# Performance work log

Hardware: AMD Instinct MI355X
Metric: run time of the kernel (lower is better)

## Reference

```python
import jax, jax.numpy as jnp
import numpy as np

B = 16384
D = 1024          # in_features
R = 64            # low_rank
E = 4             # num_experts
L = 3             # layer_num


def setup_inputs() -> dict:
    key = jax.random.key(0)
    ks = jax.random.split(key, 6)
    # xavier-normal-ish scales
    s_uv = (2.0 / (D + R)) ** 0.5
    s_c = (2.0 / (R + R)) ** 0.5
    s_g = (2.0 / (D + 1)) ** 0.5
    return {
        "inputs": jax.random.normal(ks[0], (B, D), dtype=jnp.float32),
        "U": jax.random.normal(ks[1], (L, E, D, R), dtype=jnp.float32) * s_uv,
        "V": jax.random.normal(ks[2], (L, E, D, R), dtype=jnp.float32) * s_uv,
        "C": jax.random.normal(ks[3], (L, E, R, R), dtype=jnp.float32) * s_c,
        "gate_w": jax.random.normal(ks[4], (E, D), dtype=jnp.float32) * s_g,
        "bias": jnp.zeros((L, D), dtype=jnp.float32),
    }


def reference(inputs, U, V, C, gate_w, bias):
    x0 = inputs                                  # [B, D]
    x_l = x0
    for i in range(L):
        # gating: per-expert Linear(d,1) on x_l -> [B, E], softmax over experts
        gates = jax.nn.softmax(x_l @ gate_w.T, axis=1)        # [B, E]
        # v_x = tanh(V_e^T x_l) for all experts at once
        v = jnp.tanh(jnp.einsum('bd,edr->ber', x_l, V[i]))    # [B, E, R]
        v = jnp.tanh(jnp.einsum('ers,bes->ber', C[i], v))     # [B, E, R]
        uv = jnp.einsum('edr,ber->bed', U[i], v)              # [B, E, D]
        dot = x0[:, None, :] * (uv + bias[i][None, None, :])  # [B, E, D]
        moe_out = jnp.einsum('bed,be->bd', dot, gates)        # [B, D]
        x_l = moe_out + x_l
    return x_l
```

## Files before the change

kernel.cpp:

```cpp
#include <hip/hip_runtime.h>
#include <math.h>

#define BB 16384
#define DD 1024
#define RR 64
#define EE 4
#define ER 256
#define LL 3

#define LDM 72

typedef __bf16 bf16x8 __attribute__((ext_vector_type(8)));
typedef float f32x4 __attribute__((ext_vector_type(4)));
typedef unsigned short us;

static __device__ inline us f2b(float f) {
    union { float f; unsigned u; } c; c.f = f;
    return (us)((c.u + 0x7FFF + ((c.u >> 16) & 1)) >> 16);
}
static __device__ inline float b2f(us v) {
    union { unsigned u; float f; } c; c.u = ((unsigned)v) << 16;
    return c.f;
}
static __device__ inline float fast_tanh(float x) {
    float t = __expf(2.f * x);
    return 1.f - 2.f / (t + 1.f);
}
static __device__ __forceinline__ void ld_lds16(const us* g, us* l) {
    __builtin_amdgcn_global_load_lds((const __attribute__((address_space(1))) void*)g,
                                     (__attribute__((address_space(3))) void*)l, 16, 0, 0);
}

__global__ __launch_bounds__(256) void convF2B(const float* __restrict__ s, us* __restrict__ d) {
    int f = (blockIdx.x * 256 + threadIdx.x) * 4;
    float4 v = *(const float4*)&s[f];
    *(ushort4*)&d[f] = make_ushort4(f2b(v.x), f2b(v.y), f2b(v.z), f2b(v.w));
}

__global__ __launch_bounds__(256) void convV(const float* __restrict__ V, us* __restrict__ Vt) {
    const int le = blockIdx.x;
    const int d0 = blockIdx.y * 64;
    __shared__ float t[64 * 65];
    const int tid = threadIdx.x;
    const float* Vb = V + (size_t)le * DD * RR;
    #pragma unroll
    for (int p = 0; p < 4; ++p) {
        int f = tid + p * 256; int dd = f >> 4; int c = (f & 15) * 4;
        float4 v = *(const float4*)&Vb[(size_t)(d0 + dd) * RR + c];
        t[dd * 65 + c + 0] = v.x; t[dd * 65 + c + 1] = v.y;
        t[dd * 65 + c + 2] = v.z; t[dd * 65 + c + 3] = v.w;
    }
    __syncthreads();
    int r = tid >> 2, dg = (tid & 3) * 16;
    us o[16];
    #pragma unroll
    for (int k = 0; k < 16; ++k) o[k] = f2b(t[(dg + k) * 65 + r]);
    const int l = le >> 2, eV = le & 3;
    const int row = eV * 64 + r, kt = blockIdx.y;
    us* dstL = Vt + (size_t)l * (EE * RR * DD);
    #pragma unroll
    for (int q = 0; q < 4; ++q) {
        int dd = dg + q * 4;
        int slot = ((dd >> 3) ^ row) & 7;
        *(ushort4*)&dstL[(((size_t)kt * 256 + row) * 8 + slot) * 8 + (dd & 7)] = *(ushort4*)&o[q * 4];
    }
}

__global__ __launch_bounds__(256) void convU(const float* __restrict__ U, us* __restrict__ Up) {
    int gid = blockIdx.x * 256 + threadIdx.x;
    int rb = (gid & 7) * 8;
    int d  = (gid >> 3) & 1023;
    int e  = (gid >> 13) & 3;
    int l  = gid >> 15;
    const float* s = U + (((size_t)(l * 4 + e) * 1024 + d) * 64 + rb);
    float4 v0 = *(const float4*)&s[0], v1 = *(const float4*)&s[4];
    us o[8] = { f2b(v0.x), f2b(v0.y), f2b(v0.z), f2b(v0.w),
                f2b(v1.x), f2b(v1.y), f2b(v1.z), f2b(v1.w) };
    int rh = rb >> 5, quad = (rb & 31) >> 3;
    int lane = quad * 16 + (d & 15), dblk = d >> 4;
    us* dst = Up + (size_t)l * (EE * DD * RR) + (size_t)(((e * 2 + rh) * 64 + dblk) * 64 + lane) * 8;
    *(ushort4*)&dst[0] = *(ushort4*)&o[0];
    *(ushort4*)&dst[4] = *(ushort4*)&o[4];
}

__global__ __launch_bounds__(256) void convC(const float* __restrict__ C, us* __restrict__ Cp) {
    int gid = blockIdx.x * 256 + threadIdx.x;
    int sb = (gid & 7) * 8;
    int r  = (gid >> 3) & 63;
    int e  = (gid >> 9) & 3;
    int l  = gid >> 11;
    const float* s = C + (((size_t)(l * 4 + e) * 64 + r) * 64 + sb);
    float4 v0 = *(const float4*)&s[0], v1 = *(const float4*)&s[4];
    us o[8] = { f2b(v0.x), f2b(v0.y), f2b(v0.z), f2b(v0.w),
                f2b(v1.x), f2b(v1.y), f2b(v1.z), f2b(v1.w) };
    int ks = sb >> 5, quad = (sb & 31) >> 3;
    int lane = quad * 16 + (r & 15), mt = r >> 4;
    us* dst = Cp + (size_t)l * (EE * RR * RR) + (size_t)(((e * 2 + ks) * 4 + mt) * 64 + lane) * 8;
    *(ushort4*)&dst[0] = *(ushort4*)&o[0];
    *(ushort4*)&dst[4] = *(ushort4*)&o[4];
}

__global__ __launch_bounds__(512, 2) void layer_fused(const us* __restrict__ xs,
                                                      const us* __restrict__ Vp,
                                                      const us* __restrict__ Cp,
                                                      const us* __restrict__ gwb,
                                                      const us* __restrict__ x0b,
                                                      const us* __restrict__ Up,
                                                      us* __restrict__ xbo,
                                                      const float* __restrict__ biasl,
                                                      float* __restrict__ out, int last) {
    const int row0 = blockIdx.x * 64;
    const int tid = threadIdx.x;
    const int lane = tid & 63, wave = tid >> 6;
    const int l15 = lane & 15, quad = lane >> 4;
    const int e = wave & 3, h = wave >> 2;
    const int e64 = e * 64;

    __shared__ __align__(16) union {
        struct { us buf[3][20480]; us gw[4096]; float gates[256]; } s;
        us Tt[4][64 * LDM];
        struct { us wlds[64 * 256]; float smf[8][1024]; } p2;
    } u;

    const bool gw4 = (wave < 4);
    const int r8   = lane >> 3;
    const int cA8  = (lane & 7) ^ r8;
    const int l7   = l15 & 7;

    ld_lds16(gwb + (size_t)(lane & 3) * DD + (wave * 16 + (lane >> 2)) * 8, &u.s.gw[wave * 512]);

    auto STAGE = [&](int bi, int k0) {
        us* bb = u.s.buf[bi];
        const us* vsrc = Vp + (((size_t)(k0 >> 6) * 256 + wave * 32) * 8) * 8 + lane * 8;
        #pragma unroll
        for (int j = 0; j < 4; ++j)
            ld_lds16(vsrc + j * 512, &bb[(wave * 256 + j * 64) * 8]);
        {
            int row = wave * 8 + r8;
            ld_lds16(xs + (size_t)(row0 + row) * DD + k0 + cA8 * 8, &bb[16384 + wave * 512]);
        }
    };

    f32x4 acc[4][2] = {};
    f32x4 accg = {};
    STAGE(0, 0); STAGE(1, 64);

    int cur = 0;
    for (int t = 0; t < 16; ++t) {
        if (t < 15) asm volatile("s_waitcnt vmcnt(5)" ::: "memory");
        else        asm volatile("s_waitcnt vmcnt(0)" ::: "memory");
        __builtin_amdgcn_s_barrier();
        if (t < 14) {
            int st = cur + 2; if (st >= 3) st -= 3;
            STAGE(st, (t + 2) * 64);
        }
        __builtin_amdgcn_sched_barrier(0);
        const us* bb = u.s.buf[cur];
        #pragma unroll
        for (int ks = 0; ks < 2; ++ks) {
            const int sl = ((ks * 4 + quad) ^ l7) * 8;
            bf16x8 af[4], bfr[2];
            #pragma unroll
            for (int mt = 0; mt < 4; ++mt)
                af[mt] = *(const bf16x8*)&bb[(e64 + mt * 16 + l15) * 64 + sl];
            #pragma unroll
            for (int nt = 0; nt < 2; ++nt)
                bfr[nt] = *(const bf16x8*)&bb[16384 + (h * 32 + nt * 16 + l15) * 64 + sl];
            #pragma unroll
            for (int mt = 0; mt < 4; ++mt)
                #pragma unroll
                for (int nt = 0; nt < 2; ++nt)
                    acc[mt][nt] = __builtin_amdgcn_mfma_f32_16x16x32_bf16(af[mt], bfr[nt], acc[mt][nt], 0, 0, 0);
            if (gw4) {
                bf16x8 bfrg = *(const bf16x8*)&bb[16384 + (wave * 16 + l15) * 64 + sl];
                bf16x8 afg  = *(const bf16x8*)&u.s.gw[((t * 8 + ks * 4 + quad) * 4 + (l15 & 3)) * 8];
                accg = __builtin_amdgcn_mfma_f32_16x16x32_bf16(afg, bfrg, accg, 0, 0, 0);
            }
        }
        cur = (cur == 2) ? 0 : cur + 1;
    }
    __builtin_amdgcn_s_barrier();
    __builtin_amdgcn_sched_barrier(0);

    #pragma unroll
    for (int mt = 0; mt < 4; ++mt)
        #pragma unroll
        for (int nt = 0; nt < 2; ++nt) {
            int b = h * 32 + nt * 16 + l15;
            us o[4];
            #pragma unroll
            for (int i = 0; i < 4; ++i) o[i] = f2b(fast_tanh(acc[mt][nt][i]));
            *(ushort4*)&u.Tt[e][b * LDM + mt * 16 + quad * 4] = *(ushort4*)o;
        }
    if (gw4 && quad == 0) {
        float l0 = accg[0], l1 = accg[1], l2 = accg[2], l3 = accg[3];
        float m = fmaxf(fmaxf(l0, l1), fmaxf(l2, l3));
        float g0 = __expf(l0 - m), g1 = __expf(l1 - m);
        float g2 = __expf(l2 - m), g3 = __expf(l3 - m);
        float inv = 1.f / (g0 + g1 + g2 + g3);
        int b = wave * 16 + l15;
        u.s.gates[0 * 64 + b] = g0 * inv; u.s.gates[1 * 64 + b] = g1 * inv;
        u.s.gates[2 * 64 + b] = g2 * inv; u.s.gates[3 * 64 + b] = g3 * inv;
    }
    __syncthreads();

    f32x4 acc2[4][2] = {};
    #pragma unroll
    for (int ks = 0; ks < 2; ++ks) {
        bf16x8 af2[4], bf2[2];
        #pragma unroll
        for (int mt = 0; mt < 4; ++mt)
            af2[mt] = *(const bf16x8*)&Cp[(size_t)(((e * 2 + ks) * 4 + mt) * 64 + lane) * 8];
        #pragma unroll
        for (int nt = 0; nt < 2; ++nt)
            bf2[nt] = *(const bf16x8*)&u.Tt[e][(h * 32 + nt * 16 + l15) * LDM + ks * 32 + quad * 8];
        #pragma unroll
        for (int mt = 0; mt < 4; ++mt)
            #pragma unroll
            for (int nt = 0; nt < 2; ++nt)
                acc2[mt][nt] = __builtin_amdgcn_mfma_f32_16x16x32_bf16(af2[mt], bf2[nt], acc2[mt][nt], 0, 0, 0);
    }
    __syncthreads();

    #pragma unroll
    for (int mt = 0; mt < 4; ++mt)
        #pragma unroll
        for (int nt = 0; nt < 2; ++nt) {
            int b = h * 32 + nt * 16 + l15;
            float g = u.s.gates[e64 + b];
            us o[4];
            #pragma unroll
            for (int i = 0; i < 4; ++i) o[i] = f2b(g * fast_tanh(acc2[mt][nt][i]));
            int col = e64 + mt * 16 + quad * 4;
            int cc = col >> 3, off = col & 7;
            *(ushort4*)&u.p2.wlds[b * 256 + ((cc ^ (b & 7)) << 3) + off] = *(ushort4*)o;
        }
    __syncthreads();

    const int bl = lane >> 2, dc3 = lane & 3;
    #pragma unroll 1
    for (int p = 0; p < 2; ++p) {
        const int dw = p * 512 + wave * 64;
        f32x4 pac[4][4] = {};
        bf16x8 a0[4], a1[4];
        #define LOADU(dst, S) { const int base = (S) * 64 + p * 32 + wave * 4;             \
            _Pragma("unroll")                                                              \
            for (int mt = 0; mt < 4; ++mt)                                                 \
                dst[mt] = *(const bf16x8*)&Up[(size_t)((base + mt) * 64 + lane) * 8]; }
        #define LOADW(dst, S) { const int e2 = (S) >> 1, r0q = ((S) & 1) * 32;            \
            _Pragma("unroll")                                                              \
            for (int nt = 0; nt < 4; ++nt) {                                               \
                int b = nt * 16 + l15;                                                     \
                int cc = e2 * 8 + (r0q >> 3) + quad;                                       \
                dst[nt] = *(const bf16x8*)&u.p2.wlds[b * 256 + ((cc ^ (b & 7)) << 3)];     \
            } }
        #define MM(A, W) { _Pragma("unroll")                                               \
            for (int mt = 0; mt < 4; ++mt) { _Pragma("unroll")                             \
                for (int nt = 0; nt < 4; ++nt)                                             \
                    pac[mt][nt] = __builtin_amdgcn_mfma_f32_16x16x32_bf16(A[mt], W[nt], pac[mt][nt], 0, 0, 0); } }
        LOADU(a0, 0);
        #pragma unroll
        for (int sp = 0; sp < 4; ++sp) {
            bf16x8 w0[4], w1[4];
            LOADU(a1, 2 * sp + 1);
            LOADW(w0, 2 * sp);
            MM(a0, w0);
            if (sp < 3) LOADU(a0, 2 * sp + 2);
            LOADW(w1, 2 * sp + 1);
            MM(a1, w1);
        }
        #undef LOADU
        #undef LOADW
        #undef MM

        const int dg = dw + dc3 * 16;
        uint4 X[4][2], L[4][2];
        #pragma unroll
        for (int nt = 0; nt < 4; ++nt) {
            const size_t gb = (size_t)(row0 + nt * 16 + bl) * DD + dg;
            X[nt][0] = *(const uint4*)&x0b[gb];     X[nt][1] = *(const uint4*)&x0b[gb + 8];
            L[nt][0] = *(const uint4*)&xs[gb];      L[nt][1] = *(const uint4*)&xs[gb + 8];
        }
        float bfv[16];
        *(float4*)&bfv[0]  = *(const float4*)&biasl[dg];
        *(float4*)&bfv[4]  = *(const float4*)&biasl[dg + 4];
        *(float4*)&bfv[8]  = *(const float4*)&biasl[dg + 8];
        *(float4*)&bfv[12] = *(const float4*)&biasl[dg + 12];
        float* sw = u.p2.smf[wave];
        #pragma unroll
        for (int nt = 0; nt < 4; ++nt) {
            #pragma unroll
            for (int mt = 0; mt < 4; ++mt) {
                int ch = (mt * 4 + quad) ^ (l15 & 7);
                *(f32x4*)&sw[l15 * 64 + ch * 4] = pac[mt][nt];
            }
            asm volatile("s_waitcnt lgkmcnt(0)" ::: "memory");
            __builtin_amdgcn_sched_barrier(0);
            const size_t gb = (size_t)(row0 + nt * 16 + bl) * DD + dg;
            uint xu[8], lu[8];
            *(uint4*)&xu[0] = X[nt][0]; *(uint4*)&xu[4] = X[nt][1];
            *(uint4*)&lu[0] = L[nt][0]; *(uint4*)&lu[4] = L[nt][1];
            float o[16];
            #pragma unroll
            for (int j = 0; j < 4; ++j) {
                int ch = (dc3 * 4 + j) ^ (bl & 7);
                float4 a = *(const float4*)&sw[bl * 64 + ch * 4];
                #pragma unroll
                for (int i = 0; i < 4; ++i) {
                    int k = j * 4 + i;
                    float av = (i == 0) ? a.x : (i == 1) ? a.y : (i == 2) ? a.z : a.w;
                    uint uu = xu[k >> 1], ll = lu[k >> 1];
                    float xv = b2f((k & 1) ? (us)(uu >> 16) : (us)(uu & 0xffff));
                    float xl = b2f((k & 1) ? (us)(ll >> 16) : (us)(ll & 0xffff));
                    o[k] = xv * (av + bfv[k]) + xl;
                }
            }
            if (last) {
                *(float4*)&out[gb]      = *(float4*)&o[0];
                *(float4*)&out[gb + 4]  = *(float4*)&o[4];
                *(float4*)&out[gb + 8]  = *(float4*)&o[8];
                *(float4*)&out[gb + 12] = *(float4*)&o[12];
            } else {
                us ob[16];
                #pragma unroll
                for (int k = 0; k < 16; ++k) ob[k] = f2b(o[k]);
                *(uint4*)&xbo[gb]     = *(uint4*)&ob[0];
                *(uint4*)&xbo[gb + 8] = *(uint4*)&ob[8];
            }
        }
    }
}

extern "C" void kernel_launch(void* const* d_in, const int* in_sizes, int n_in,
                              void* d_out, int out_size, void* d_ws, size_t ws_size,
                              hipStream_t stream) {
    const float* inputs = (const float*)d_in[0];
    const float* U      = (const float*)d_in[1];
    const float* V      = (const float*)d_in[2];
    const float* C      = (const float*)d_in[3];
    const float* gw     = (const float*)d_in[4];
    const float* bias   = (const float*)d_in[5];
    float* out = (float*)d_out;

    us* xb0 = (us*)d_ws;
    us* xb  = xb0 + (size_t)BB * DD;
    us* gwb = xb + (size_t)BB * DD;
    us* Vp  = gwb + (size_t)EE * DD;
    us* Up  = Vp + (size_t)LL * EE * RR * DD;
    us* Cp  = Up + (size_t)LL * EE * DD * RR;

    convF2B<<<dim3(BB * DD / 1024), 256, 0, stream>>>(inputs, xb0);
    convU<<<dim3(LL * EE * DD * RR / 8 / 256), 256, 0, stream>>>(U, Up);
    convC<<<dim3(LL * EE * RR * RR / 8 / 256), 256, 0, stream>>>(C, Cp);
    convF2B<<<dim3(EE * DD / 1024), 256, 0, stream>>>(gw, gwb);
    convV<<<dim3(LL * EE, DD / 64), 256, 0, stream>>>(V, Vp);

    for (int i = 0; i < LL; ++i) {
        const us* xs = (i == 0) ? xb0 : xb;
        layer_fused<<<dim3(BB / 64), 512, 0, stream>>>(
            xs, Vp + (size_t)i * EE * RR * DD, Cp + (size_t)i * EE * RR * RR, gwb,
            xb0, Up + (size_t)i * EE * DD * RR, xb, bias + (size_t)i * DD,
            out, i == LL - 1);
    }
}
```

Baseline: 262.3 us.

## Fuse all three layers into one kernel keeping x_l tile resident in LDS

Replaces the three per-layer launches with a single kernel in which each block keeps its 64-row bf16 x_l tile (128KB) in shared memory across all layers. The V weights and gate weights are pre-packed into MFMA fragment order and read straight from global memory, not staged through LDS. This removes the per-layer global round trip of x_l, two kernel launches, and the software-pipelined LDS staging. In exchange, the large LDS footprint limits occupancy to one block per CU, and V loads are unpipelined global reads that may stall the MFMA loop.

```diff
diff --git a/kernel.cpp b/kernel.cpp
--- a/kernel.cpp
+++ b/kernel.cpp
@@ -8,8 +8,6 @@
 #define ER 256
 #define LL 3
 
-#define LDM 72
-
 typedef __bf16 bf16x8 __attribute__((ext_vector_type(8)));
 typedef float f32x4 __attribute__((ext_vector_type(4)));
 typedef unsigned short us;
@@ -37,7 +35,7 @@
     *(ushort4*)&d[f] = make_ushort4(f2b(v.x), f2b(v.y), f2b(v.z), f2b(v.w));
 }
 
-__global__ __launch_bounds__(256) void convV(const float* __restrict__ V, us* __restrict__ Vt) {
+__global__ __launch_bounds__(256) void convVq(const float* __restrict__ V, us* __restrict__ Vq) {
     const int le = blockIdx.x;
     const int d0 = blockIdx.y * 64;
     __shared__ float t[64 * 65];
@@ -56,14 +54,15 @@
     #pragma unroll
     for (int k = 0; k < 16; ++k) o[k] = f2b(t[(dg + k) * 65 + r]);
     const int l = le >> 2, eV = le & 3;
-    const int row = eV * 64 + r, kt = blockIdx.y;
-    us* dstL = Vt + (size_t)l * (EE * RR * DD);
-    #pragma unroll
-    for (int q = 0; q < 4; ++q) {
-        int dd = dg + q * 4;
-        int slot = ((dd >> 3) ^ row) & 7;
-        *(ushort4*)&dstL[(((size_t)kt * 256 + row) * 8 + slot) * 8 + (dd & 7)] = *(ushort4*)&o[q * 4];
-    }
+    const int mt = r >> 4, l15r = r & 15;
+    const int s = (d0 + dg) >> 5, q0 = (dg >> 3) & 3;
+    us* dstL = Vq + (size_t)l * (EE * RR * DD);
+    size_t g0 = ((size_t)((eV * 4 + mt) * 32 + s) * 64 + q0 * 16 + l15r) * 8;
+    size_t g1 = ((size_t)((eV * 4 + mt) * 32 + s) * 64 + (q0 + 1) * 16 + l15r) * 8;
+    *(ushort4*)&dstL[g0 + 0] = *(ushort4*)&o[0];
+    *(ushort4*)&dstL[g0 + 4] = *(ushort4*)&o[4];
+    *(ushort4*)&dstL[g1 + 0] = *(ushort4*)&o[8];
+    *(ushort4*)&dstL[g1 + 4] = *(ushort4*)&o[12];
 }
 
 __global__ __launch_bounds__(256) void convU(const float* __restrict__ U, us* __restrict__ Up) {
@@ -100,234 +99,210 @@
     *(ushort4*)&dst[4] = *(ushort4*)&o[4];
 }
 
-__global__ __launch_bounds__(512, 2) void layer_fused(const us* __restrict__ xs,
-                                                      const us* __restrict__ Vp,
-                                                      const us* __restrict__ Cp,
-                                                      const us* __restrict__ gwb,
-                                                      const us* __restrict__ x0b,
-                                                      const us* __restrict__ Up,
-                                                      us* __restrict__ xbo,
-                                                      const float* __restrict__ biasl,
-                                                      float* __restrict__ out, int last) {
+__global__ __launch_bounds__(256) void convGq(const float* __restrict__ gw, us* __restrict__ gq) {
+    int idx = blockIdx.x * 256 + threadIdx.x;
+    int s = idx >> 6, lane = idx & 63;
+    int quad = lane >> 4, l15 = lane & 15;
+    us o[8];
+    #pragma unroll
+    for (int i = 0; i < 8; ++i)
+        o[i] = (l15 < 4) ? f2b(gw[(size_t)l15 * DD + s * 32 + quad * 8 + i]) : (us)0;
+    *(ushort4*)&gq[(size_t)idx * 8 + 0] = *(ushort4*)&o[0];
+    *(ushort4*)&gq[(size_t)idx * 8 + 4] = *(ushort4*)&o[4];
+}
+
+__global__ __launch_bounds__(512, 1) void meganet(const us* __restrict__ xb0,
+                                                  const us* __restrict__ Vq,
+                                                  const us* __restrict__ Cp,
+                                                  const us* __restrict__ gq,
+                                                  const us* __restrict__ Up,
+                                                  const float* __restrict__ bias,
+                                                  float* __restrict__ out) {
     const int row0 = blockIdx.x * 64;
     const int tid = threadIdx.x;
     const int lane = tid & 63, wave = tid >> 6;
     const int l15 = lane & 15, quad = lane >> 4;
     const int e = wave & 3, h = wave >> 2;
-    const int e64 = e * 64;
-
-    __shared__ __align__(16) union {
-        struct { us buf[3][20480]; us gw[4096]; float gates[256]; } s;
-        us Tt[4][64 * LDM];
-        struct { us wlds[64 * 256]; float smf[8][1024]; } p2;
-    } u;
-
-    const bool gw4 = (wave < 4);
-    const int r8   = lane >> 3;
-    const int cA8  = (lane & 7) ^ r8;
-    const int l7   = l15 & 7;
-
-    ld_lds16(gwb + (size_t)(lane & 3) * DD + (wave * 16 + (lane >> 2)) * 8, &u.s.gw[wave * 512]);
-
-    auto STAGE = [&](int bi, int k0) {
-        us* bb = u.s.buf[bi];
-        const us* vsrc = Vp + (((size_t)(k0 >> 6) * 256 + wave * 32) * 8) * 8 + lane * 8;
+
+    __shared__ __align__(16) us xtile[65536];
+    __shared__ __align__(16) us regA[16384];
+
+    {
+        const int r8 = lane >> 3, c = lane & 7;
+        const us* src0 = xb0 + (size_t)(row0 + wave * 8 + r8) * DD + ((c ^ r8) * 8);
         #pragma unroll
-        for (int j = 0; j < 4; ++j)
-            ld_lds16(vsrc + j * 512, &bb[(wave * 256 + j * 64) * 8]);
+        for (int kt = 0; kt < 16; ++kt)
+            ld_lds16(src0 + kt * 64, &xtile[(size_t)(kt * 64 + wave * 8) * 64]);
+        asm volatile("s_waitcnt vmcnt(0)" ::: "memory");
+    }
+    __syncthreads();
+
+    for (int l = 0; l < LL; ++l) {
+        const us* Vl = Vq + (size_t)l * (EE * RR * DD);
+        const us* Cl = Cp + (size_t)l * (EE * RR * RR);
+        const us* Ul = Up + (size_t)l * (EE * DD * RR);
+        const float* bl = bias + (size_t)l * DD;
+        const int lastl = (l == LL - 1);
+
+        f32x4 acc[4][2] = {};
+        f32x4 ag0 = {}, ag1 = {};
+        const int b0 = h * 32 + l15, b1 = h * 32 + 16 + l15;
+        const int s0 = (b0 & 7), s1 = (b1 & 7);
+        #pragma unroll 4
+        for (int t = 0; t < 16; ++t) {
+            #pragma unroll
+            for (int ks = 0; ks < 2; ++ks) {
+                const int s = t * 2 + ks;
+                bf16x8 A[4], B[2], G;
+                #pragma unroll
+                for (int mt = 0; mt < 4; ++mt)
+                    A[mt] = *(const bf16x8*)&Vl[(size_t)(((e * 4 + mt) * 32 + s) * 64 + lane) * 8];
+                B[0] = *(const bf16x8*)&xtile[(size_t)((t * 64 + b0) * 8 + ((ks * 4 + quad) ^ s0)) * 8];
+                B[1] = *(const bf16x8*)&xtile[(size_t)((t * 64 + b1) * 8 + ((ks * 4 + quad) ^ s1)) * 8];
+                G    = *(const bf16x8*)&gq[(size_t)(s * 64 + lane) * 8];
+                #pragma unroll
+                for (int mt = 0; mt < 4; ++mt) {
+                    acc[mt][0] = __builtin_amdgcn_mfma_f32_16x16x32_bf16(A[mt], B[0], acc[mt][0], 0, 0, 0);
+                    acc[mt][1] = __builtin_amdgcn_mfma_f32_16x16x32_bf16(A[mt], B[1], acc[mt][1], 0, 0, 0);
+                }
+                ag0 = __builtin_amdgcn_mfma_f32_16x16x32_bf16(G, B[0], ag0, 0, 0, 0);
+                ag1 = __builtin_amdgcn_mfma_f32_16x16x32_bf16(G, B[1], ag1, 0, 0, 0);
+            }
+        }
+
+        float g0b, g1b;
         {
-            int row = wave * 8 + r8;
-            ld_lds16(xs + (size_t)(row0 + row) * DD + k0 + cA8 * 8, &bb[16384 + wave * 512]);
+            float m0 = fmaxf(fmaxf(ag0[0], ag0[1]), fmaxf(ag0[2], ag0[3]));
+            float x0e = __expf(ag0[0] - m0), x1e = __expf(ag0[1] - m0);
+            float x2e = __expf(ag0[2] - m0), x3e = __expf(ag0[3] - m0);
+            float inv0 = 1.f / (x0e + x1e + x2e + x3e);
+            float ge0 = ((e == 0) ? x0e : (e == 1) ? x1e : (e == 2) ? x2e : x3e) * inv0;
+            float m1 = fmaxf(fmaxf(ag1[0], ag1[1]), fmaxf(ag1[2], ag1[3]));
+            float y0e = __expf(ag1[0] - m1), y1e = __expf(ag1[1] - m1);
+            float y2e = __expf(ag1[2] - m1), y3e = __expf(ag1[3] - m1);
+            float inv1 = 1.f / (y0e + y1e + y2e + y3e);
+            float ge1 = ((e == 0) ? y0e : (e == 1) ? y1e : (e == 2) ? y2e : y3e) * inv1;
+            g0b = __shfl(ge0, l15, 64);
+            g1b = __shfl(ge1, l15, 64);
         }
-    };
-
-    f32x4 acc[4][2] = {};
-    f32x4 accg = {};
-    STAGE(0, 0); STAGE(1, 64);
-
-    int cur = 0;
-    for (int t = 0; t < 16; ++t) {
-        if (t < 15) asm volatile("s_waitcnt vmcnt(5)" ::: "memory");
-        else        asm volatile("s_waitcnt vmcnt(0)" ::: "memory");
-        __builtin_amdgcn_s_barrier();
-        if (t < 14) {
-            int st = cur + 2; if (st >= 3) st -= 3;
-            STAGE(st, (t + 2) * 64);
-        }
-        __builtin_amdgcn_sched_barrier(0);
-        const us* bb = u.s.buf[cur];
+
+        us* Tt_e = regA + e * 4096;
+        #pragma unroll
+        for (int mt = 0; mt < 4; ++mt)
+            #pragma unroll
+            for (int nt = 0; nt < 2; ++nt) {
+                int b = h * 32 + nt * 16 + l15;
+                int rc = mt * 2 + (quad >> 1);
+                us o[4];
+                #pragma unroll
+                for (int i = 0; i < 4; ++i) o[i] = f2b(fast_tanh(acc[mt][nt][i]));
+                *(ushort4*)&Tt_e[b * 64 + ((rc ^ (b & 7)) << 3) + (quad & 1) * 4] = *(ushort4*)o;
+            }
+
+        f32x4 acc2[4][2] = {};
         #pragma unroll
         for (int ks = 0; ks < 2; ++ks) {
-            const int sl = ((ks * 4 + quad) ^ l7) * 8;
-            bf16x8 af[4], bfr[2];
+            bf16x8 af2[4], bf2[2];
             #pragma unroll
             for (int mt = 0; mt < 4; ++mt)
-                af[mt] = *(const bf16x8*)&bb[(e64 + mt * 16 + l15) * 64 + sl];
-            #pragma unroll
-            for (int nt = 0; nt < 2; ++nt)
-                bfr[nt] = *(const bf16x8*)&bb[16384 + (h * 32 + nt * 16 + l15) * 64 + sl];
+                af2[mt] = *(const bf16x8*)&Cl[(size_t)(((e * 2 + ks) * 4 + mt) * 64 + lane) * 8];
+            #pragma unroll
+            for (int nt = 0; nt < 2; ++nt) {
+                int b = h * 32 + nt * 16 + l15;
+                int rc = ks * 4 + quad;
+                bf2[nt] = *(const bf16x8*)&Tt_e[b * 64 + ((rc ^ (b & 7)) << 3)];
+            }
             #pragma unroll
             for (int mt = 0; mt < 4; ++mt)
                 #pragma unroll
                 for (int nt = 0; nt < 2; ++nt)
-                    acc[mt][nt] = __builtin_amdgcn_mfma_f32_16x16x32_bf16(af[mt], bfr[nt], acc[mt][nt], 0, 0, 0);
-            if (gw4) {
-                bf16x8 bfrg = *(const bf16x8*)&bb[16384 + (wave * 16 + l15) * 64 + sl];
-                bf16x8 afg  = *(const bf16x8*)&u.s.gw[((t * 8 + ks * 4 + quad) * 4 + (l15 & 3)) * 8];
-                accg = __builtin_amdgcn_mfma_f32_16x16x32_bf16(afg, bfrg, accg, 0, 0, 0);
-            }
+                    acc2[mt][nt] = __builtin_amdgcn_mfma_f32_16x16x32_bf16(af2[mt], bf2[nt], acc2[mt][nt], 0, 0, 0);
         }
-        cur = (cur == 2) ? 0 : cur + 1;
-    }
-    __builtin_amdgcn_s_barrier();
-    __builtin_amdgcn_sched_barrier(0);
-
-    #pragma unroll
-    for (int mt = 0; mt < 4; ++mt)
-        #pragma unroll
-        for (int nt = 0; nt < 2; ++nt) {
-            int b = h * 32 + nt * 16 + l15;
-            us o[4];
-            #pragma unroll
-            for (int i = 0; i < 4; ++i) o[i] = f2b(fast_tanh(acc[mt][nt][i]));
-            *(ushort4*)&u.Tt[e][b * LDM + mt * 16 + quad * 4] = *(ushort4*)o;
-        }
-    if (gw4 && quad == 0) {
-        float l0 = accg[0], l1 = accg[1], l2 = accg[2], l3 = accg[3];
-        float m = fmaxf(fmaxf(l0, l1), fmaxf(l2, l3));
-        float g0 = __expf(l0 - m), g1 = __expf(l1 - m);
-        float g2 = __expf(l2 - m), g3 = __expf(l3 - m);
-        float inv = 1.f / (g0 + g1 + g2 + g3);
-        int b = wave * 16 + l15;
-        u.s.gates[0 * 64 + b] = g0 * inv; u.s.gates[1 * 64 + b] = g1 * inv;
-        u.s.gates[2 * 64 + b] = g2 * inv; u.s.gates[3 * 64 + b] = g3 * inv;
-    }
-    __syncthreads();
-
-    f32x4 acc2[4][2] = {};
-    #pragma unroll
-    for (int ks = 0; ks < 2; ++ks) {
-        bf16x8 af2[4], bf2[2];
+        __syncthreads();
+
         #pragma unroll
         for (int mt = 0; mt < 4; ++mt)
-            af2[mt] = *(const bf16x8*)&Cp[(size_t)(((e * 2 + ks) * 4 + mt) * 64 + lane) * 8];
-        #pragma unroll
-        for (int nt = 0; nt < 2; ++nt)
-            bf2[nt] = *(const bf16x8*)&u.Tt[e][(h * 32 + nt * 16 + l15) * LDM + ks * 32 + quad * 8];
-        #pragma unroll
-        for (int mt = 0; mt < 4; ++mt)
-            #pragma unroll
-            for (int nt = 0; nt < 2; ++nt)
-                acc2[mt][nt] = __builtin_amdgcn_mfma_f32_16x16x32_bf16(af2[mt], bf2[nt], acc2[mt][nt], 0, 0, 0);
-    }
-    __syncthreads();
-
-    #pragma unroll
-    for (int mt = 0; mt < 4; ++mt)
-        #pragma unroll
-        for (int nt = 0; nt < 2; ++nt) {
-            int b = h * 32 + nt * 16 + l15;
-            float g = u.s.gates[e64 + b];
-            us o[4];
-            #pragma unroll
-            for (int i = 0; i < 4; ++i) o[i] = f2b(g * fast_tanh(acc2[mt][nt][i]));
-            int col = e64 + mt * 16 + quad * 4;
-            int cc = col >> 3, off = col & 7;
-            *(ushort4*)&u.p2.wlds[b * 256 + ((cc ^ (b & 7)) << 3) + off] = *(ushort4*)o;
+            #pragma unroll
+            for (int nt = 0; nt < 2; ++nt) {
+                int b = h * 32 + nt * 16 + l15;
+                float g = nt ? g1b : g0b;
+                us o[4];
+                #pragma unroll
+                for (int i = 0; i < 4; ++i) o[i] = f2b(g * fast_tanh(acc2[mt][nt][i]));
+                int col = e * 64 + mt * 16 + quad * 4;
+                int cc = col >> 3, off = col & 7;
+                *(ushort4*)&regA[b * 256 + ((cc ^ (b & 7)) << 3) + off] = *(ushort4*)o;
+            }
+        __syncthreads();
+
+        #pragma unroll 1
+        for (int p = 0; p < 2; ++p) {
+            const int dw = p * 512 + wave * 64;
+            f32x4 pac[4][4] = {};
+            bf16x8 a0[4], a1[4];
+            #define LOADU(dst, S) { const int base = (S) * 64 + p * 32 + wave * 4;             \
+                _Pragma("unroll")                                                              \
+                for (int mt = 0; mt < 4; ++mt)                                                 \
+                    dst[mt] = *(const bf16x8*)&Ul[(size_t)((base + mt) * 64 + lane) * 8]; }
+            #define LOADW(dst, S) { const int e2 = (S) >> 1, r0q = ((S) & 1) * 32;             \
+                _Pragma("unroll")                                                              \
+                for (int nt = 0; nt < 4; ++nt) {                                               \
+                    int b = nt * 16 + l15;                                                     \
+                    int cc = e2 * 8 + (r0q >> 3) + quad;                                       \
+                    dst[nt] = *(const bf16x8*)&regA[b * 256 + ((cc ^ (b & 7)) << 3)];          \
+                } }
+            #define MM(A, W) { _Pragma("unroll")                                               \
+                for (int mt = 0; mt < 4; ++mt) { _Pragma("unroll")                             \
+                    for (int nt = 0; nt < 4; ++nt)                                             \
+                        pac[mt][nt] = __builtin_amdgcn_mfma_f32_16x16x32_bf16(A[mt], W[nt], pac[mt][nt], 0, 0, 0); } }
+            LOADU(a0, 0);
+            #pragma unroll
+            for (int sp = 0; sp < 4; ++sp) {
+                bf16x8 w0[4], w1[4];
+                LOADU(a1, 2 * sp + 1);
+                LOADW(w0, 2 * sp);
+                MM(a0, w0);
+                if (sp < 3) LOADU(a0, 2 * sp + 2);
+                LOADW(w1, 2 * sp + 1);
+                MM(a1, w1);
+            }
+            #undef LOADU
+            #undef LOADW
+            #undef MM
+
+            ushort4 X[4][4];
+            #pragma unroll
+            for (int nt = 0; nt < 4; ++nt)
+                #pragma unroll
+                for (int mt = 0; mt < 4; ++mt)
+                    X[nt][mt] = *(const ushort4*)&xb0[(size_t)(row0 + nt * 16 + l15) * DD + dw + mt * 16 + quad * 4];
+            float bfv[4][4];
+            #pragma unroll
+            for (int mt = 0; mt < 4; ++mt)
+                *(float4*)&bfv[mt][0] = *(const float4*)&bl[dw + mt * 16 + quad * 4];
+
+            #pragma unroll
+            for (int nt = 0; nt < 4; ++nt)
+                #pragma unroll
+                for (int mt = 0; mt < 4; ++mt) {
+                    const int b = nt * 16 + l15;
+                    const int d = dw + mt * 16 + quad * 4;
+                    const int slot = (((d >> 3) & 7) ^ (b & 7));
+                    us* xl_p = &xtile[(size_t)(((d >> 6) * 64 + b) * 8 + slot) * 8 + (quad & 1) * 4];
+                    ushort4 xl4 = *(ushort4*)xl_p;
+                    float o[4];
+                    o[0] = b2f(X[nt][mt].x) * (pac[mt][nt][0] + bfv[mt][0]) + b2f(xl4.x);
+                    o[1] = b2f(X[nt][mt].y) * (pac[mt][nt][1] + bfv[mt][1]) + b2f(xl4.y);
+                    o[2] = b2f(X[nt][mt].z) * (pac[mt][nt][2] + bfv[mt][2]) + b2f(xl4.z);
+                    o[3] = b2f(X[nt][mt].w) * (pac[mt][nt][3] + bfv[mt][3]) + b2f(xl4.w);
+                    if (lastl) {
+                        *(float4*)&out[(size_t)(row0 + b) * DD + d] = make_float4(o[0], o[1], o[2], o[3]);
+                    } else {
+                        *(ushort4*)xl_p = make_ushort4(f2b(o[0]), f2b(o[1]), f2b(o[2]), f2b(o[3]));
+                    }
+                }
         }
-    __syncthreads();
-
-    const int bl = lane >> 2, dc3 = lane & 3;
-    #pragma unroll 1
-    for (int p = 0; p < 2; ++p) {
-        const int dw = p * 512 + wave * 64;
-        f32x4 pac[4][4] = {};
-        bf16x8 a0[4], a1[4];
-        #define LOADU(dst, S) { const int base = (S) * 64 + p * 32 + wave * 4;             \
-            _Pragma("unroll")                                                              \
-            for (int mt = 0; mt < 4; ++mt)                                                 \
-                dst[mt] = *(const bf16x8*)&Up[(size_t)((base + mt) * 64 + lane) * 8]; }
-        #define LOADW(dst, S) { const int e2 = (S) >> 1, r0q = ((S) & 1) * 32;            \
-            _Pragma("unroll")                                                              \
-            for (int nt = 0; nt < 4; ++nt) {                                               \
-                int b = nt * 16 + l15;                                                     \
-                int cc = e2 * 8 + (r0q >> 3) + quad;                                       \
-                dst[nt] = *(const bf16x8*)&u.p2.wlds[b * 256 + ((cc ^ (b & 7)) << 3)];     \
-            } }
-        #define MM(A, W) { _Pragma("unroll")                                               \
-            for (int mt = 0; mt < 4; ++mt) { _Pragma("unroll")                             \
-                for (int nt = 0; nt < 4; ++nt)                                             \
-                    pac[mt][nt] = __builtin_amdgcn_mfma_f32_16x16x32_bf16(A[mt], W[nt], pac[mt][nt], 0, 0, 0); } }
-        LOADU(a0, 0);
-        #pragma unroll
-        for (int sp = 0; sp < 4; ++sp) {
-            bf16x8 w0[4], w1[4];
-            LOADU(a1, 2 * sp + 1);
-            LOADW(w0, 2 * sp);
-            MM(a0, w0);
-            if (sp < 3) LOADU(a0, 2 * sp + 2);
-            LOADW(w1, 2 * sp + 1);
-            MM(a1, w1);
-        }
-        #undef LOADU
-        #undef LOADW
-        #undef MM
-
-        const int dg = dw + dc3 * 16;
-        uint4 X[4][2], L[4][2];
-        #pragma unroll
-        for (int nt = 0; nt < 4; ++nt) {
-            const size_t gb = (size_t)(row0 + nt * 16 + bl) * DD + dg;
-            X[nt][0] = *(const uint4*)&x0b[gb];     X[nt][1] = *(const uint4*)&x0b[gb + 8];
-            L[nt][0] = *(const uint4*)&xs[gb];      L[nt][1] = *(const uint4*)&xs[gb + 8];
-        }
-        float bfv[16];
-        *(float4*)&bfv[0]  = *(const float4*)&biasl[dg];
-        *(float4*)&bfv[4]  = *(const float4*)&biasl[dg + 4];
-        *(float4*)&bfv[8]  = *(const float4*)&biasl[dg + 8];
-        *(float4*)&bfv[12] = *(const float4*)&biasl[dg + 12];
-        float* sw = u.p2.smf[wave];
-        #pragma unroll
-        for (int nt = 0; nt < 4; ++nt) {
-            #pragma unroll
-            for (int mt = 0; mt < 4; ++mt) {
-                int ch = (mt * 4 + quad) ^ (l15 & 7);
-                *(f32x4*)&sw[l15 * 64 + ch * 4] = pac[mt][nt];
-            }
-            asm volatile("s_waitcnt lgkmcnt(0)" ::: "memory");
-            __builtin_amdgcn_sched_barrier(0);
-            const size_t gb = (size_t)(row0 + nt * 16 + bl) * DD + dg;
-            uint xu[8], lu[8];
-            *(uint4*)&xu[0] = X[nt][0]; *(uint4*)&xu[4] = X[nt][1];
-            *(uint4*)&lu[0] = L[nt][0]; *(uint4*)&lu[4] = L[nt][1];
-            float o[16];
-            #pragma unroll
-            for (int j = 0; j < 4; ++j) {
-                int ch = (dc3 * 4 + j) ^ (bl & 7);
-                float4 a = *(const float4*)&sw[bl * 64 + ch * 4];
-                #pragma unroll
-                for (int i = 0; i < 4; ++i) {
-                    int k = j * 4 + i;
-                    float av = (i == 0) ? a.x : (i == 1) ? a.y : (i == 2) ? a.z : a.w;
-                    uint uu = xu[k >> 1], ll = lu[k >> 1];
-                    float xv = b2f((k & 1) ? (us)(uu >> 16) : (us)(uu & 0xffff));
-                    float xl = b2f((k & 1) ? (us)(ll >> 16) : (us)(ll & 0xffff));
-                    o[k] = xv * (av + bfv[k]) + xl;
-                }
-            }
-            if (last) {
-                *(float4*)&out[gb]      = *(float4*)&o[0];
-                *(float4*)&out[gb + 4]  = *(float4*)&o[4];
-                *(float4*)&out[gb + 8]  = *(float4*)&o[8];
-                *(float4*)&out[gb + 12] = *(float4*)&o[12];
-            } else {
-                us ob[16];
-                #pragma unroll
-                for (int k = 0; k < 16; ++k) ob[k] = f2b(o[k]);
-                *(uint4*)&xbo[gb]     = *(uint4*)&ob[0];
-                *(uint4*)&xbo[gb + 8] = *(uint4*)&ob[8];
-            }
-        }
+        if (!lastl) __syncthreads();
     }
 }
 
@@ -343,23 +318,16 @@
     float* out = (float*)d_out;
 
     us* xb0 = (us*)d_ws;
-    us* xb  = xb0 + (size_t)BB * DD;
-    us* gwb = xb + (size_t)BB * DD;
-    us* Vp  = gwb + (size_t)EE * DD;
-    us* Up  = Vp + (size_t)LL * EE * RR * DD;
+    us* Vq  = xb0 + (size_t)BB * DD;
+    us* Up  = Vq + (size_t)LL * EE * RR * DD;
     us* Cp  = Up + (size_t)LL * EE * DD * RR;
+    us* gqp = Cp + (size_t)LL * EE * RR * RR;
 
     convF2B<<<dim3(BB * DD / 1024), 256, 0, stream>>>(inputs, xb0);
     convU<<<dim3(LL * EE * DD * RR / 8 / 256), 256, 0, stream>>>(U, Up);
     convC<<<dim3(LL * EE * RR * RR / 8 / 256), 256, 0, stream>>>(C, Cp);
-    convF2B<<<dim3(EE * DD / 1024), 256, 0, stream>>>(gw, gwb);
-    convV<<<dim3(LL * EE, DD / 64), 256, 0, stream>>>(V, Vp);
-
-    for (int i = 0; i < LL; ++i) {
-        const us* xs = (i == 0) ? xb0 : xb;
-        layer_fused<<<dim3(BB / 64), 512, 0, stream>>>(
-            xs, Vp + (size_t)i * EE * RR * DD, Cp + (size_t)i * EE * RR * RR, gwb,
-            xb0, Up + (size_t)i * EE * DD * RR, xb, bias + (size_t)i * DD,
-            out, i == LL - 1);
-    }
-}
+    convGq<<<dim3(8), 256, 0, stream>>>(gw, gqp);
+    convVq<<<dim3(LL * EE, DD / 64), 256, 0, stream>>>(V, Vq);
+
+    meganet<<<dim3(BB / 64), 512, 0, stream>>>(xb0, Vq, Cp, gqp, Up, bias, out);
+}
```

New measurement: 341.2 us. 1.3x slower.
